# Kernel optimization log

Hardware: AMD Instinct MI355X
Metric: run time of the kernel (lower is better)

The kernel has to match this reference:

```python
import jax, jax.numpy as jnp
import numpy as np

N_USERS = 19968
N_ITEMS = 6144
EMBED = 64
V_DIM = 4096
T_DIM = 384
KNN_K = 10
LAMBDA = 0.9          # lambda_coeff
N_LAYERS = 1          # item-graph propagation layers
N_UI_LAYERS = 2       # len(weight_size)
NNZ = 600000


def build_sim(x):
    # cosine similarity: row-normalize then x @ x.T  -> [N, N]
    xn = x / jnp.linalg.norm(x, axis=-1, keepdims=True)
    return xn @ xn.T


def knn_graph(adj, k):
    # torch.topk + scatter_: keep top-k values per row, zeros elsewhere
    vals, idx = jax.lax.top_k(adj, k)                      # [N, k]
    rows = jnp.arange(adj.shape[0])[:, None]
    return jnp.zeros_like(adj).at[rows, idx].set(vals)


def norm_laplacian(adj):
    # D^{-1/2} A D^{-1/2} with inf -> 0
    d = jnp.sum(adj, axis=-1) ** -0.5
    d = jnp.where(jnp.isinf(d), 0.0, d)
    return adj * d[:, None] * d[None, :]


def setup_inputs() -> dict:
    key = jax.random.key(0)
    ks = jax.random.split(key, 10)
    user_emb = jax.random.normal(ks[0], (N_USERS, EMBED), jnp.float32) * 0.1
    item_emb = jax.random.normal(ks[1], (N_ITEMS, EMBED), jnp.float32) * 0.1
    image_feat = jax.random.normal(ks[2], (N_ITEMS, V_DIM), jnp.float32)
    text_feat = jax.random.normal(ks[3], (N_ITEMS, T_DIM), jnp.float32)
    image_trs_w = jax.random.normal(ks[4], (V_DIM, EMBED), jnp.float32) * 0.02
    image_trs_b = jnp.zeros((EMBED,), jnp.float32)
    text_trs_w = jax.random.normal(ks[5], (T_DIM, EMBED), jnp.float32) * 0.05
    text_trs_b = jnp.zeros((EMBED,), jnp.float32)
    modal_weight = jnp.array([0.5, 0.5], jnp.float32)
    # frozen buffers: knn laplacians built from the raw multimodal features
    image_orig_adj = norm_laplacian(knn_graph(build_sim(image_feat), KNN_K))
    text_orig_adj = norm_laplacian(knn_graph(build_sim(text_feat), KNN_K))
    n_nodes = N_USERS + N_ITEMS
    rows = jax.random.randint(ks[6], (NNZ,), 0, n_nodes, dtype=jnp.int32)
    cols = jax.random.randint(ks[7], (NNZ,), 0, n_nodes, dtype=jnp.int32)
    adj_indices = jnp.stack([rows, cols], axis=0)           # [2, NNZ] COO
    adj_values = jax.random.uniform(ks[8], (NNZ,), jnp.float32) * 0.01
    return {
        "user_emb": user_emb, "item_emb": item_emb,
        "image_feat": image_feat, "text_feat": text_feat,
        "image_trs_w": image_trs_w, "image_trs_b": image_trs_b,
        "text_trs_w": text_trs_w, "text_trs_b": text_trs_b,
        "modal_weight": modal_weight,
        "image_orig_adj": image_orig_adj, "text_orig_adj": text_orig_adj,
        "adj_indices": adj_indices, "adj_values": adj_values,
        "knn_k": KNN_K,
    }


def reference(user_emb, item_emb, image_feat, text_feat,
              image_trs_w, image_trs_b, text_trs_w, text_trs_b,
              modal_weight, image_orig_adj, text_orig_adj,
              adj_indices, adj_values, knn_k):
    # modality projections
    image_feats = image_feat @ image_trs_w + image_trs_b   # [N_items, 64]
    text_feats = text_feat @ text_trs_w + text_trs_b       # [N_items, 64]
    w = jax.nn.softmax(modal_weight)
    # build_item_graph=True branch
    image_adj = knn_graph(build_sim(image_feats), knn_k)
    text_adj = knn_graph(build_sim(text_feats), knn_k)
    learned_adj = norm_laplacian(w[0] * image_adj + w[1] * text_adj)
    original_adj = w[0] * image_orig_adj + w[1] * text_orig_adj
    item_adj = (1.0 - LAMBDA) * learned_adj + LAMBDA * original_adj
    # item-graph propagation
    h = item_emb
    for _ in range(N_LAYERS):
        h = item_adj @ h
    # lightgcn user-item propagation via sparse COO matmul
    ego = jnp.concatenate([user_emb, item_emb], axis=0)    # [n_nodes, 64]
    n_nodes = ego.shape[0]
    src, dst = adj_indices[0], adj_indices[1]
    all_emb = [ego]
    for _ in range(N_UI_LAYERS):
        ego = jax.ops.segment_sum(adj_values[:, None] * ego[dst], src,
                                  num_segments=n_nodes)
        all_emb.append(ego)
    all_emb = jnp.mean(jnp.stack(all_emb, axis=1), axis=1)
    u_g = all_emb[:N_USERS]
    h_norm = h / jnp.maximum(jnp.linalg.norm(h, axis=1, keepdims=True), 1e-12)
    i_g = all_emb[N_USERS:] + h_norm
    return u_g, i_g
```

## Files before the change

### kernel.cpp

```cpp
#include <hip/hip_runtime.h>
#include <hip/hip_bf16.h>

#define NU 19968
#define NI 6144
#define NNODE (NU + NI)
#define EMB 64
#define VD 4096
#define TD 384
#define NNZE 600000
#define LAMB 0.9f
#define NCH 8
#define CPC (NI / NCH)
#define MAXC 16

typedef __attribute__((ext_vector_type(8))) short bf16x8;
typedef __attribute__((ext_vector_type(4))) float f32x4;
#define MFMA16(a, b, c) __builtin_amdgcn_mfma_f32_16x16x32_bf16(a, b, c, 0, 0, 0)


__device__ __forceinline__ void vins(float (&cv)[10], float v) {
#pragma unroll
    for (int s = 0; s < 10; ++s) {
        float mx = fmaxf(cv[s], v);
        v = fminf(cv[s], v);
        cv[s] = mx;
    }
}

__device__ __forceinline__ void topk_ins_tie(float (&cv)[10], int (&ci)[10], float v, int j) {
#pragma unroll
    for (int s = 0; s < 10; ++s) {
        bool take = (v > cv[s]) || (v == cv[s] && j < ci[s]);
        if (take) {
            float tv = cv[s]; cv[s] = v; v = tv;
            int tj = ci[s]; ci[s] = j; j = tj;
        }
    }
}

__device__ __forceinline__ float2 softmax2(const float* mw) {
    float e0 = expf(mw[0]), e1 = expf(mw[1]);
    float inv = 1.0f / (e0 + e1);
    return make_float2(e0 * inv, e1 * inv);
}

__device__ __forceinline__ unsigned short f2bf(float f) {
    unsigned int u = __float_as_uint(f);
    unsigned int r = (u + 0x7FFFu + ((u >> 16) & 1u)) >> 16;
    return (unsigned short)r;
}
__device__ __forceinline__ float bf2f(unsigned short h) { return __uint_as_float(((unsigned int)h) << 16); }

__device__ __forceinline__ f32x4 sim_tile(const unsigned short* __restrict__ xh,
                                          const unsigned short* __restrict__ xl,
                                          bf16x8 ahi0, bf16x8 ahi1, bf16x8 alo0, bf16x8 alo1,
                                          int c, int fq) {
    const size_t bbase = (size_t)c * 64 + fq * 8;
    bf16x8 bhi0 = *(const bf16x8*)(xh + bbase);
    bf16x8 bhi1 = *(const bf16x8*)(xh + bbase + 32);
    bf16x8 blo0 = *(const bf16x8*)(xl + bbase);
    bf16x8 blo1 = *(const bf16x8*)(xl + bbase + 32);
    f32x4 a = {0.f, 0.f, 0.f, 0.f};
    a = MFMA16(ahi0, bhi0, a);
    a = MFMA16(ahi1, bhi1, a);
    a = MFMA16(ahi0, blo0, a);
    a = MFMA16(ahi1, blo1, a);
    a = MFMA16(alo0, bhi0, a);
    a = MFMA16(alo1, bhi1, a);
    return a;
}


__global__ __launch_bounds__(256) void gemm_tr(const float* __restrict__ A, const float* __restrict__ W,
                                               float* __restrict__ C, int M, int K, int kps) {
    __shared__ float At[64][64];
    __shared__ float Wt[64][64];
    const int t = threadIdx.x;
    const int m0 = blockIdx.x * 64;
    const int k0 = blockIdx.y * kps;
    const int tm = t & 15, tn = t >> 4;
    float acc[4][4] = {};
    for (int kt = k0; kt < k0 + kps; kt += 64) {
        __syncthreads();
        for (int i = t; i < 1024; i += 256) {
            int m = i >> 4, k4 = (i & 15) << 2;
            float4 v = *(const float4*)(A + (size_t)(m0 + m) * K + kt + k4);
            At[k4 + 0][m] = v.x; At[k4 + 1][m] = v.y; At[k4 + 2][m] = v.z; At[k4 + 3][m] = v.w;
        }
        for (int i = t; i < 1024; i += 256) {
            int kk = i >> 4, n4 = (i & 15) << 2;
            *(float4*)&Wt[kk][n4] = *(const float4*)(W + (size_t)(kt + kk) * 64 + n4);
        }
        __syncthreads();
#pragma unroll
        for (int kk = 0; kk < 64; ++kk) {
            float a[4], b[4];
            *(float4*)a = *(const float4*)&At[kk][tm << 2];
            *(float4*)b = *(const float4*)&Wt[kk][tn << 2];
#pragma unroll
            for (int i = 0; i < 4; ++i)
#pragma unroll
                for (int j = 0; j < 4; ++j) acc[i][j] += a[i] * b[j];
        }
    }
#pragma unroll
    for (int i = 0; i < 4; ++i)
#pragma unroll
        for (int j = 0; j < 4; ++j)
            unsafeAtomicAdd(&C[(size_t)(m0 + (tm << 2) + i) * 64 + (tn << 2) + j], acc[i][j]);
}


__global__ __launch_bounds__(256) void rownorm(const float* __restrict__ C, const float* __restrict__ bias,
                                               unsigned short* __restrict__ xh, unsigned short* __restrict__ xl) {
    int row = blockIdx.x * 4 + (threadIdx.x >> 6);
    int lane = threadIdx.x & 63;
    float v = C[(size_t)row * 64 + lane] + bias[lane];
    float ss = v * v;
#pragma unroll
    for (int o = 32; o; o >>= 1) ss += __shfl_xor(ss, o, 64);
    float xn = v * (1.0f / sqrtf(ss));
    unsigned short h = f2bf(xn);
    float lo = xn - bf2f(h);
    xh[(size_t)row * 64 + lane] = h;
    xl[(size_t)row * 64 + lane] = f2bf(lo);
}


__global__ __launch_bounds__(256) void sims_tauA(const unsigned short* __restrict__ xh_img,
                                                 const unsigned short* __restrict__ xl_img,
                                                 const unsigned short* __restrict__ xh_txt,
                                                 const unsigned short* __restrict__ xl_txt,
                                                 float* __restrict__ tkv) {
    const unsigned short* xh = blockIdx.z ? xh_txt : xh_img;
    const unsigned short* xl = blockIdx.z ? xl_txt : xl_img;
    const int r0 = blockIdx.x * 64;
    const int c0 = blockIdx.y * CPC;
    const int t = threadIdx.x;
    const int wave = t >> 6, lane = t & 63;
    const int fr = lane & 15, fq = lane >> 4;

    const size_t abase = (size_t)(r0 + wave * 16 + fr) * 64 + fq * 8;
    bf16x8 ahi0 = *(const bf16x8*)(xh + abase);
    bf16x8 ahi1 = *(const bf16x8*)(xh + abase + 32);
    bf16x8 alo0 = *(const bf16x8*)(xl + abase);
    bf16x8 alo1 = *(const bf16x8*)(xl + abase + 32);

    float cv[4][10];
#pragma unroll
    for (int r = 0; r < 4; ++r)
#pragma unroll
        for (int s = 0; s < 10; ++s) cv[r][s] = -INFINITY;

    for (int ct = 0; ct < CPC / 64; ++ct) {
        const int cbase = c0 + ct * 64;
#pragma unroll
        for (int cs = 0; cs < 4; ++cs) {
            f32x4 a = sim_tile(xh, xl, ahi0, ahi1, alo0, alo1, cbase + cs * 16 + fr, fq);
#pragma unroll
            for (int r = 0; r < 4; ++r)
                if (a[r] > cv[r][9]) vins(cv[r], a[r]);
        }
    }

#pragma unroll
    for (int m = 1; m <= 8; m <<= 1) {
#pragma unroll
        for (int r = 0; r < 4; ++r) {
            float ov[10];
#pragma unroll
            for (int s = 0; s < 10; ++s) ov[s] = __shfl_xor(cv[r][s], m);
            bool done = false;
#pragma unroll
            for (int s = 0; s < 10; ++s) {
                if (!done) {
                    if (__all(ov[s] <= cv[r][9])) done = true;
                    else if (ov[s] > cv[r][9]) vins(cv[r], ov[s]);
                }
            }
        }
    }

    if (fr == 0) {
#pragma unroll
        for (int r = 0; r < 4; ++r) {
            int row = r0 + wave * 16 + fq * 4 + r;
            size_t base = ((size_t)(blockIdx.z * NI + row) * NCH + blockIdx.y) * 10;
#pragma unroll
            for (int s = 0; s < 10; ++s) tkv[base + s] = cv[r][s];
        }
    }
}


__global__ void tau_merge(const float* __restrict__ tkv, float* __restrict__ tau) {
    int g = blockIdx.x * blockDim.x + threadIdx.x;
    if (g >= 2 * NI) return;
    float cv[10];
#pragma unroll
    for (int s = 0; s < 10; ++s) cv[s] = -INFINITY;
    for (int u = 0; u < NCH * 10; ++u) {
        float v = tkv[(size_t)g * NCH * 10 + u];
        if (v > cv[9]) vins(cv, v);
    }
    tau[g] = cv[9];
}


__global__ __launch_bounds__(256) void sims_collect(const unsigned short* __restrict__ xh_img,
                                                    const unsigned short* __restrict__ xl_img,
                                                    const unsigned short* __restrict__ xh_txt,
                                                    const unsigned short* __restrict__ xl_txt,
                                                    const float* __restrict__ tau,
                                                    int* __restrict__ ccnt,
                                                    float* __restrict__ cval, int* __restrict__ ccol) {
    const unsigned short* xh = blockIdx.z ? xh_txt : xh_img;
    const unsigned short* xl = blockIdx.z ? xl_txt : xl_img;
    const int r0 = blockIdx.x * 64;
    const int c0 = blockIdx.y * CPC;
    const int t = threadIdx.x;
    const int wave = t >> 6, lane = t & 63;
    const int fr = lane & 15, fq = lane >> 4;

    const size_t abase = (size_t)(r0 + wave * 16 + fr) * 64 + fq * 8;
    bf16x8 ahi0 = *(const bf16x8*)(xh + abase);
    bf16x8 ahi1 = *(const bf16x8*)(xh + abase + 32);
    bf16x8 alo0 = *(const bf16x8*)(xl + abase);
    bf16x8 alo1 = *(const bf16x8*)(xl + abase + 32);

    float tv[4];
    int grow[4];
#pragma unroll
    for (int r = 0; r < 4; ++r) {
        grow[r] = blockIdx.z * NI + r0 + wave * 16 + fq * 4 + r;
        tv[r] = tau[grow[r]];
    }

    for (int ct = 0; ct < CPC / 64; ++ct) {
        const int cbase = c0 + ct * 64;
#pragma unroll
        for (int cs = 0; cs < 4; ++cs) {
            const int c = cbase + cs * 16 + fr;
            f32x4 a = sim_tile(xh, xl, ahi0, ahi1, alo0, alo1, c, fq);
#pragma unroll
            for (int r = 0; r < 4; ++r) {
                if (a[r] >= tv[r]) {
                    int p = atomicAdd(&ccnt[grow[r]], 1);
                    if (p < MAXC) {
                        cval[(size_t)grow[r] * MAXC + p] = a[r];
                        ccol[(size_t)grow[r] * MAXC + p] = c;
                    }
                }
            }
        }
    }
}


__global__ void topk_cand(const int* __restrict__ ccnt, const float* __restrict__ cval,
                          const int* __restrict__ ccol,
                          float* __restrict__ fvv, int* __restrict__ fii) {
    int g = blockIdx.x * blockDim.x + threadIdx.x;
    if (g >= 2 * NI) return;
    float cv[10]; int ci[10];
#pragma unroll
    for (int s = 0; s < 10; ++s) { cv[s] = -INFINITY; ci[s] = 0x7fffffff; }
    int n = ccnt[g]; if (n > MAXC) n = MAXC;
    for (int u = 0; u < n; ++u)
        topk_ins_tie(cv, ci, cval[(size_t)g * MAXC + u], ccol[(size_t)g * MAXC + u]);
#pragma unroll
    for (int s = 0; s < 10; ++s) { fvv[(size_t)g * 10 + s] = cv[s]; fii[(size_t)g * 10 + s] = ci[s]; }
}


__global__ void calc_dinv(const float* __restrict__ fvv, const float* __restrict__ mw, float* __restrict__ dinv) {
    int i = blockIdx.x * blockDim.x + threadIdx.x;
    if (i >= NI) return;
    float2 w = softmax2(mw);
    float s = 0.f;
    for (int u = 0; u < 10; ++u) s += w.x * fvv[(size_t)i * 10 + u];
    for (int u = 0; u < 10; ++u) s += w.y * fvv[(size_t)(NI + i) * 10 + u];
    dinv[i] = (s > 0.f) ? (1.0f / sqrtf(s)) : 0.f;
}


__global__ __launch_bounds__(256) void compute_h(const float* __restrict__ img_o, const float* __restrict__ txt_o,
                                                 const float* __restrict__ item_emb,
                                                 const float* __restrict__ fvv, const int* __restrict__ fii,
                                                 const float* __restrict__ dinv, const float* __restrict__ mw,
                                                 float* __restrict__ hnorm) {
    const int i = blockIdx.x;
    const int t = threadIdx.x;
    __shared__ int   sj[64];
    __shared__ float sc[64];
    __shared__ int   scnt;
    __shared__ float part[4][64];
    if (t == 0) scnt = 0;
    __syncthreads();
    float2 w = softmax2(mw);
    const float4* ro = (const float4*)(img_o + (size_t)i * NI);
    const float4* to = (const float4*)(txt_o + (size_t)i * NI);
    for (int u = t; u < NI / 4; u += 256) {
        float4 a = ro[u], b = to[u];
        float c[4] = { w.x * a.x + w.y * b.x, w.x * a.y + w.y * b.y,
                       w.x * a.z + w.y * b.z, w.x * a.w + w.y * b.w };
#pragma unroll
        for (int q = 0; q < 4; ++q)
            if (c[q] != 0.f) { int p = atomicAdd(&scnt, 1); sj[p] = u * 4 + q; sc[p] = LAMB * c[q]; }
    }
    if (t < 20) {
        int m = t / 10, s = t % 10;
        float v = fvv[((size_t)m * NI + i) * 10 + s];
        int   j = fii[((size_t)m * NI + i) * 10 + s];
        float wm = m ? w.y : w.x;
        float c = (1.0f - LAMB) * wm * v * dinv[i] * dinv[j];
        int p = atomicAdd(&scnt, 1); sj[p] = j; sc[p] = c;
    }
    __syncthreads();
    const int cnt = scnt;
    const int dim = t & 63, q = t >> 6;
    float acc = 0.f;
    for (int e = q; e < cnt; e += 4) acc += sc[e] * item_emb[(size_t)sj[e] * 64 + dim];
    part[q][dim] = acc;
    __syncthreads();
    if (t < 64) {
        float h = part[0][t] + part[1][t] + part[2][t] + part[3][t];
        float ss = h * h;
#pragma unroll
        for (int o = 32; o; o >>= 1) ss += __shfl_xor(ss, o, 64);
        float scale = 1.0f / fmaxf(sqrtf(ss), 1e-12f);
        hnorm[(size_t)i * 64 + t] = h * scale;
    }
}


__global__ void hist_k(const int* __restrict__ aidx, int* __restrict__ cnt) {
    int e = blockIdx.x * 256 + threadIdx.x;
    if (e < NNZE) atomicAdd(&cnt[aidx[e]], 1);
}

__global__ void scan_partial(const int* __restrict__ cnt, int* __restrict__ rp, int* __restrict__ partials) {
    __shared__ int sm[256];
    int t = threadIdx.x;
    int i = blockIdx.x * 256 + t;
    int v = cnt[i];
    sm[t] = v;
    __syncthreads();
    for (int o = 1; o < 256; o <<= 1) {
        int x = (t >= o) ? sm[t - o] : 0;
        __syncthreads();
        sm[t] += x;
        __syncthreads();
    }
    rp[i] = sm[t] - v;
    if (t == 255) partials[blockIdx.x] = sm[255];
}

__global__ void scan_totals(int* __restrict__ partials, int* __restrict__ rp) {
    if (threadIdx.x == 0) {
        int s = 0;
        for (int b = 0; b < NNODE / 256; ++b) { int v = partials[b]; partials[b] = s; s += v; }
        rp[NNODE] = s;
    }
}

__global__ void add_off(int* __restrict__ rp, const int* __restrict__ partials, int* __restrict__ fill) {
    int i = blockIdx.x * 256 + threadIdx.x;
    int v = rp[i] + partials[blockIdx.x];
    rp[i] = v;
    fill[i] = v;
}

__global__ void scatter_k(const int* __restrict__ aidx, const float* __restrict__ avals,
                          int* __restrict__ fill, int* __restrict__ cdst, float* __restrict__ cval) {
    int e = blockIdx.x * 256 + threadIdx.x;
    if (e >= NNZE) return;
    int src = aidx[e];
    int p = atomicAdd(&fill[src], 1);
    cdst[p] = aidx[NNZE + e];
    cval[p] = avals[e];
}


__global__ __launch_bounds__(256) void ui_gather(const float* __restrict__ uin, const float* __restrict__ iin,
                                                 const float* __restrict__ full_in,
                                                 const int* __restrict__ rp, const int* __restrict__ cdst,
                                                 const float* __restrict__ cval, float* __restrict__ out) {
    int row = blockIdx.x * 4 + (threadIdx.x >> 6);
    int lane = threadIdx.x & 63;
    int s = rp[row], e = rp[row + 1];
    float acc = 0.f;
    int p = s;
    for (; p + 2 <= e; p += 2) {
        int d0 = cdst[p], d1 = cdst[p + 1];
        float v0 = cval[p], v1 = cval[p + 1];
        const float* r0 = full_in ? full_in + (size_t)d0 * 64
                                  : (d0 < NU ? uin + (size_t)d0 * 64 : iin + (size_t)(d0 - NU) * 64);
        const float* r1 = full_in ? full_in + (size_t)d1 * 64
                                  : (d1 < NU ? uin + (size_t)d1 * 64 : iin + (size_t)(d1 - NU) * 64);
        acc += v0 * r0[lane];
        acc += v1 * r1[lane];
    }
    if (p < e) {
        int d0 = cdst[p]; float v0 = cval[p];
        const float* r0 = full_in ? full_in + (size_t)d0 * 64
                                  : (d0 < NU ? uin + (size_t)d0 * 64 : iin + (size_t)(d0 - NU) * 64);
        acc += v0 * r0[lane];
    }
    out[(size_t)row * 64 + lane] = acc;
}


__global__ __launch_bounds__(256) void final_out(const float* __restrict__ ue, const float* __restrict__ ie,
                                                 const float* __restrict__ e1, const float* __restrict__ e2,
                                                 const float* __restrict__ hnorm, float* __restrict__ out) {
    int g = blockIdx.x * 256 + threadIdx.x;
    if (g >= NNODE * 16) return;
    int n = g >> 4;
    float4 a = (n < NU) ? ((const float4*)ue)[g] : ((const float4*)ie)[g - NU * 16];
    float4 b = ((const float4*)e1)[g];
    float4 c = ((const float4*)e2)[g];
    const float third = 1.0f / 3.0f;
    float4 r;
    r.x = (a.x + b.x + c.x) * third;
    r.y = (a.y + b.y + c.y) * third;
    r.z = (a.z + b.z + c.z) * third;
    r.w = (a.w + b.w + c.w) * third;
    if (n >= NU) {
        float4 h = ((const float4*)hnorm)[g - NU * 16];
        r.x += h.x; r.y += h.y; r.z += h.z; r.w += h.w;
    }
    ((float4*)out)[g] = r;
}


extern "C" void kernel_launch(void* const* d_in, const int* in_sizes, int n_in,
                              void* d_out, int out_size, void* d_ws, size_t ws_size,
                              hipStream_t stream) {
    const float* user_emb   = (const float*)d_in[0];
    const float* item_emb   = (const float*)d_in[1];
    const float* image_feat = (const float*)d_in[2];
    const float* text_feat  = (const float*)d_in[3];
    const float* img_w      = (const float*)d_in[4];
    const float* img_b      = (const float*)d_in[5];
    const float* txt_w      = (const float*)d_in[6];
    const float* txt_b      = (const float*)d_in[7];
    const float* mw         = (const float*)d_in[8];
    const float* img_orig   = (const float*)d_in[9];
    const float* txt_orig   = (const float*)d_in[10];
    const int*   aidx       = (const int*)d_in[11];
    const float* avals      = (const float*)d_in[12];

    float* C_img = (float*)d_ws;
    float* C_txt = C_img + (size_t)NI * EMB;
    unsigned short* xh_img = (unsigned short*)(C_txt + (size_t)NI * EMB);
    unsigned short* xl_img = xh_img + (size_t)NI * EMB;
    unsigned short* xh_txt = xl_img + (size_t)NI * EMB;
    unsigned short* xl_txt = xh_txt + (size_t)NI * EMB;
    float* tkvA    = (float*)(xl_txt + (size_t)NI * EMB);
    float* tau     = tkvA + (size_t)2 * NI * NCH * 10;
    int*   ccnt    = (int*)(tau + 2 * NI);
    float* candv   = (float*)(ccnt + 2 * NI);
    int*   candc   = (int*)(candv + (size_t)2 * NI * MAXC);
    float* fin_val = (float*)(candc + (size_t)2 * NI * MAXC);
    int*   fin_idx = (int*)(fin_val + 2 * NI * 10);
    float* dinv    = (float*)(fin_idx + 2 * NI * 10);
    float* hnorm   = dinv + NI;
    float* ego1    = hnorm + (size_t)NI * EMB;
    float* ego2    = ego1 + (size_t)NNODE * EMB;
    int* cnt      = (int*)(ego2 + (size_t)NNODE * EMB);
    int* row_ptr  = cnt + NNODE;
    int* fill     = row_ptr + NNODE + 1;
    int* partials = fill + NNODE;
    int* csr_dst  = partials + 128;
    float* csr_val = (float*)(csr_dst + NNZE);

    hipMemsetAsync(C_img, 0, (size_t)NI * EMB * 4, stream);
    hipMemsetAsync(C_txt, 0, (size_t)NI * EMB * 4, stream);
    hipMemsetAsync(cnt, 0, (size_t)NNODE * 4, stream);
    hipMemsetAsync(ccnt, 0, (size_t)2 * NI * 4, stream);

    hist_k<<<(NNZE + 255) / 256, 256, 0, stream>>>(aidx, cnt);
    scan_partial<<<NNODE / 256, 256, 0, stream>>>(cnt, row_ptr, partials);
    scan_totals<<<1, 64, 0, stream>>>(partials, row_ptr);
    add_off<<<NNODE / 256, 256, 0, stream>>>(row_ptr, partials, fill);
    scatter_k<<<(NNZE + 255) / 256, 256, 0, stream>>>(aidx, avals, fill, csr_dst, csr_val);

    gemm_tr<<<dim3(NI / 64, 8), 256, 0, stream>>>(image_feat, img_w, C_img, NI, VD, VD / 8);
    gemm_tr<<<dim3(NI / 64, 6), 256, 0, stream>>>(text_feat,  txt_w, C_txt, NI, TD, TD / 6);

    rownorm<<<NI / 4, 256, 0, stream>>>(C_img, img_b, xh_img, xl_img);
    rownorm<<<NI / 4, 256, 0, stream>>>(C_txt, txt_b, xh_txt, xl_txt);

    sims_tauA<<<dim3(NI / 64, NCH, 2), 256, 0, stream>>>(xh_img, xl_img, xh_txt, xl_txt, tkvA);
    tau_merge<<<(2 * NI + 255) / 256, 256, 0, stream>>>(tkvA, tau);
    sims_collect<<<dim3(NI / 64, NCH, 2), 256, 0, stream>>>(xh_img, xl_img, xh_txt, xl_txt,
                                                            tau, ccnt, candv, candc);
    topk_cand<<<(2 * NI + 255) / 256, 256, 0, stream>>>(ccnt, candv, candc, fin_val, fin_idx);

    calc_dinv<<<(NI + 255) / 256, 256, 0, stream>>>(fin_val, mw, dinv);

    compute_h<<<NI, 256, 0, stream>>>(img_orig, txt_orig, item_emb, fin_val, fin_idx, dinv, mw, hnorm);

    ui_gather<<<NNODE / 4, 256, 0, stream>>>(user_emb, item_emb, nullptr, row_ptr, csr_dst, csr_val, ego1);
    ui_gather<<<NNODE / 4, 256, 0, stream>>>(user_emb, item_emb, ego1,    row_ptr, csr_dst, csr_val, ego2);

    final_out<<<(NNODE * 16 + 255) / 256, 256, 0, stream>>>(user_emb, item_emb, ego1, ego2, hnorm, (float*)d_out);
}
```

Measured before the change: 1.034 ms.

## Use split-bf16 MFMA projection GEMM, vectorize sparse gather, parallelize scan

Replaces the fp32 FMA projection GEMM with an MFMA kernel that splits inputs into bf16 hi/lo parts and computes three products. Each K-split now writes its own partial buffer that rownorm sums, which removes the atomics and memsets. The sparse user-item gather uses float4 loads across four edge groups with a shuffle reduction, and the serial scan_totals becomes a shared-memory parallel scan. It also doubles the similarity column chunks (NCH) and aliases workspace buffers, at the cost of slightly lower GEMM precision and more tau-merge work.

```diff
diff --git a/kernel.cpp b/kernel.cpp
--- a/kernel.cpp
+++ b/kernel.cpp
@@ -9,7 +9,7 @@
 #define TD 384
 #define NNZE 600000
 #define LAMB 0.9f
-#define NCH 8
+#define NCH 16
 #define CPC (NI / NCH)
 #define MAXC 16
 
@@ -71,51 +71,75 @@
 }
 
 
-__global__ __launch_bounds__(256) void gemm_tr(const float* __restrict__ A, const float* __restrict__ W,
-                                               float* __restrict__ C, int M, int K, int kps) {
-    __shared__ float At[64][64];
-    __shared__ float Wt[64][64];
+__global__ __launch_bounds__(256) void gemm_mfma(const float* __restrict__ A, const float* __restrict__ W,
+                                                 float* __restrict__ Cp, int K, int kps) {
+    __shared__ unsigned short Ah[64][72], Al[64][72], Wh[64][72], Wl[64][72];
     const int t = threadIdx.x;
     const int m0 = blockIdx.x * 64;
     const int k0 = blockIdx.y * kps;
-    const int tm = t & 15, tn = t >> 4;
-    float acc[4][4] = {};
+    const int wv = t >> 6, lane = t & 63;
+    const int fr = lane & 15, fq = lane >> 4;
+    f32x4 acc[4] = {{0,0,0,0},{0,0,0,0},{0,0,0,0},{0,0,0,0}};
     for (int kt = k0; kt < k0 + kps; kt += 64) {
         __syncthreads();
-        for (int i = t; i < 1024; i += 256) {
+#pragma unroll
+        for (int q = 0; q < 4; ++q) {
+            int i = t + 256 * q;
             int m = i >> 4, k4 = (i & 15) << 2;
             float4 v = *(const float4*)(A + (size_t)(m0 + m) * K + kt + k4);
-            At[k4 + 0][m] = v.x; At[k4 + 1][m] = v.y; At[k4 + 2][m] = v.z; At[k4 + 3][m] = v.w;
-        }
-        for (int i = t; i < 1024; i += 256) {
+            float f[4] = {v.x, v.y, v.z, v.w};
+#pragma unroll
+            for (int j = 0; j < 4; ++j) {
+                unsigned short h = f2bf(f[j]);
+                Ah[m][k4 + j] = h;
+                Al[m][k4 + j] = f2bf(f[j] - bf2f(h));
+            }
+        }
+#pragma unroll
+        for (int q = 0; q < 4; ++q) {
+            int i = t + 256 * q;
             int kk = i >> 4, n4 = (i & 15) << 2;
-            *(float4*)&Wt[kk][n4] = *(const float4*)(W + (size_t)(kt + kk) * 64 + n4);
+            float4 v = *(const float4*)(W + (size_t)(kt + kk) * 64 + n4);
+            float f[4] = {v.x, v.y, v.z, v.w};
+#pragma unroll
+            for (int j = 0; j < 4; ++j) {
+                unsigned short h = f2bf(f[j]);
+                Wh[n4 + j][kk] = h;
+                Wl[n4 + j][kk] = f2bf(f[j] - bf2f(h));
+            }
         }
         __syncthreads();
 #pragma unroll
-        for (int kk = 0; kk < 64; ++kk) {
-            float a[4], b[4];
-            *(float4*)a = *(const float4*)&At[kk][tm << 2];
-            *(float4*)b = *(const float4*)&Wt[kk][tn << 2];
-#pragma unroll
-            for (int i = 0; i < 4; ++i)
-#pragma unroll
-                for (int j = 0; j < 4; ++j) acc[i][j] += a[i] * b[j];
-        }
-    }
-#pragma unroll
-    for (int i = 0; i < 4; ++i)
-#pragma unroll
-        for (int j = 0; j < 4; ++j)
-            unsafeAtomicAdd(&C[(size_t)(m0 + (tm << 2) + i) * 64 + (tn << 2) + j], acc[i][j]);
-}
-
-
-__global__ __launch_bounds__(256) void rownorm(const float* __restrict__ C, const float* __restrict__ bias,
-                                               unsigned short* __restrict__ xh, unsigned short* __restrict__ xl) {
+        for (int k2 = 0; k2 < 2; ++k2) {
+            bf16x8 ah = *(const bf16x8*)&Ah[wv * 16 + fr][k2 * 32 + fq * 8];
+            bf16x8 al = *(const bf16x8*)&Al[wv * 16 + fr][k2 * 32 + fq * 8];
+#pragma unroll
+            for (int cs = 0; cs < 4; ++cs) {
+                bf16x8 wh = *(const bf16x8*)&Wh[cs * 16 + fr][k2 * 32 + fq * 8];
+                bf16x8 wl = *(const bf16x8*)&Wl[cs * 16 + fr][k2 * 32 + fq * 8];
+                acc[cs] = MFMA16(ah, wh, acc[cs]);
+                acc[cs] = MFMA16(ah, wl, acc[cs]);
+                acc[cs] = MFMA16(al, wh, acc[cs]);
+            }
+        }
+    }
+    const size_t base = (size_t)blockIdx.y * NI * 64;
+#pragma unroll
+    for (int cs = 0; cs < 4; ++cs)
+#pragma unroll
+        for (int r = 0; r < 4; ++r)
+            Cp[base + (size_t)(m0 + wv * 16 + fq * 4 + r) * 64 + cs * 16 + fr] = acc[cs][r];
+}
+
+
+__global__ __launch_bounds__(256) void rownorm(const float* __restrict__ Cp, const float* __restrict__ bias,
+                                               unsigned short* __restrict__ xh, unsigned short* __restrict__ xl,
+                                               int ns) {
     int row = blockIdx.x * 4 + (threadIdx.x >> 6);
     int lane = threadIdx.x & 63;
-    float v = C[(size_t)row * 64 + lane] + bias[lane];
+    float v = 0.f;
+    for (int s = 0; s < ns; ++s) v += Cp[((size_t)s * NI + row) * 64 + lane];
+    v += bias[lane];
     float ss = v * v;
 #pragma unroll
     for (int o = 32; o; o >>= 1) ss += __shfl_xor(ss, o, 64);
@@ -357,11 +381,20 @@
 }
 
 __global__ void scan_totals(int* __restrict__ partials, int* __restrict__ rp) {
-    if (threadIdx.x == 0) {
-        int s = 0;
-        for (int b = 0; b < NNODE / 256; ++b) { int v = partials[b]; partials[b] = s; s += v; }
-        rp[NNODE] = s;
-    }
+    __shared__ int sm[128];
+    int t = threadIdx.x;
+    const int NB = NNODE / 256;
+    int v = (t < NB) ? partials[t] : 0;
+    sm[t] = v;
+    __syncthreads();
+    for (int o = 1; o < 128; o <<= 1) {
+        int x = (t >= o) ? sm[t - o] : 0;
+        __syncthreads();
+        sm[t] += x;
+        __syncthreads();
+    }
+    if (t < NB) partials[t] = sm[t] - v;
+    if (t == 127) rp[NNODE] = sm[127];
 }
 
 __global__ void add_off(int* __restrict__ rp, const int* __restrict__ partials, int* __restrict__ fill) {
@@ -388,26 +421,25 @@
                                                  const float* __restrict__ cval, float* __restrict__ out) {
     int row = blockIdx.x * 4 + (threadIdx.x >> 6);
     int lane = threadIdx.x & 63;
+    int g16 = lane & 15, egrp = lane >> 4;
     int s = rp[row], e = rp[row + 1];
-    float acc = 0.f;
-    int p = s;
-    for (; p + 2 <= e; p += 2) {
-        int d0 = cdst[p], d1 = cdst[p + 1];
-        float v0 = cval[p], v1 = cval[p + 1];
-        const float* r0 = full_in ? full_in + (size_t)d0 * 64
-                                  : (d0 < NU ? uin + (size_t)d0 * 64 : iin + (size_t)(d0 - NU) * 64);
-        const float* r1 = full_in ? full_in + (size_t)d1 * 64
-                                  : (d1 < NU ? uin + (size_t)d1 * 64 : iin + (size_t)(d1 - NU) * 64);
-        acc += v0 * r0[lane];
-        acc += v1 * r1[lane];
-    }
-    if (p < e) {
-        int d0 = cdst[p]; float v0 = cval[p];
-        const float* r0 = full_in ? full_in + (size_t)d0 * 64
-                                  : (d0 < NU ? uin + (size_t)d0 * 64 : iin + (size_t)(d0 - NU) * 64);
-        acc += v0 * r0[lane];
-    }
-    out[(size_t)row * 64 + lane] = acc;
+    float4 acc = {0.f, 0.f, 0.f, 0.f};
+    for (int p = s + egrp; p < e; p += 4) {
+        int d = cdst[p];
+        float v = cval[p];
+        const float* r0 = full_in ? full_in + (size_t)d * 64
+                                  : (d < NU ? uin + (size_t)d * 64 : iin + (size_t)(d - NU) * 64);
+        float4 x = *(const float4*)(r0 + g16 * 4);
+        acc.x += v * x.x; acc.y += v * x.y; acc.z += v * x.z; acc.w += v * x.w;
+    }
+#pragma unroll
+    for (int m = 16; m <= 32; m <<= 1) {
+        acc.x += __shfl_xor(acc.x, m, 64);
+        acc.y += __shfl_xor(acc.y, m, 64);
+        acc.z += __shfl_xor(acc.z, m, 64);
+        acc.w += __shfl_xor(acc.w, m, 64);
+    }
+    if (egrp == 0) *(float4*)(out + (size_t)row * 64 + g16 * 4) = acc;
 }
 
 
@@ -451,14 +483,19 @@
     const int*   aidx       = (const int*)d_in[11];
     const float* avals      = (const float*)d_in[12];
 
-    float* C_img = (float*)d_ws;
-    float* C_txt = C_img + (size_t)NI * EMB;
-    unsigned short* xh_img = (unsigned short*)(C_txt + (size_t)NI * EMB);
+    float* R = (float*)d_ws;
+    float* Cp_img = R;
+    float* Cp_txt = R + 3145728;
+    float* tkvA   = R + 3145728 + 2359296;
+    float* ego1   = R;
+    float* ego2   = R + 1671168;
+
+    float* after = R + 7471104;
+    unsigned short* xh_img = (unsigned short*)after;
     unsigned short* xl_img = xh_img + (size_t)NI * EMB;
     unsigned short* xh_txt = xl_img + (size_t)NI * EMB;
     unsigned short* xl_txt = xh_txt + (size_t)NI * EMB;
-    float* tkvA    = (float*)(xl_txt + (size_t)NI * EMB);
-    float* tau     = tkvA + (size_t)2 * NI * NCH * 10;
+    float* tau     = (float*)(xl_txt + (size_t)NI * EMB);
     int*   ccnt    = (int*)(tau + 2 * NI);
     float* candv   = (float*)(ccnt + 2 * NI);
     int*   candc   = (int*)(candv + (size_t)2 * NI * MAXC);
@@ -466,31 +503,27 @@
     int*   fin_idx = (int*)(fin_val + 2 * NI * 10);
     float* dinv    = (float*)(fin_idx + 2 * NI * 10);
     float* hnorm   = dinv + NI;
-    float* ego1    = hnorm + (size_t)NI * EMB;
-    float* ego2    = ego1 + (size_t)NNODE * EMB;
-    int* cnt      = (int*)(ego2 + (size_t)NNODE * EMB);
+    int* cnt      = (int*)(hnorm + (size_t)NI * EMB);
     int* row_ptr  = cnt + NNODE;
     int* fill     = row_ptr + NNODE + 1;
     int* partials = fill + NNODE;
     int* csr_dst  = partials + 128;
     float* csr_val = (float*)(csr_dst + NNZE);
 
-    hipMemsetAsync(C_img, 0, (size_t)NI * EMB * 4, stream);
-    hipMemsetAsync(C_txt, 0, (size_t)NI * EMB * 4, stream);
     hipMemsetAsync(cnt, 0, (size_t)NNODE * 4, stream);
     hipMemsetAsync(ccnt, 0, (size_t)2 * NI * 4, stream);
 
     hist_k<<<(NNZE + 255) / 256, 256, 0, stream>>>(aidx, cnt);
     scan_partial<<<NNODE / 256, 256, 0, stream>>>(cnt, row_ptr, partials);
-    scan_totals<<<1, 64, 0, stream>>>(partials, row_ptr);
+    scan_totals<<<1, 128, 0, stream>>>(partials, row_ptr);
     add_off<<<NNODE / 256, 256, 0, stream>>>(row_ptr, partials, fill);
     scatter_k<<<(NNZE + 255) / 256, 256, 0, stream>>>(aidx, avals, fill, csr_dst, csr_val);
 
-    gemm_tr<<<dim3(NI / 64, 8), 256, 0, stream>>>(image_feat, img_w, C_img, NI, VD, VD / 8);
-    gemm_tr<<<dim3(NI / 64, 6), 256, 0, stream>>>(text_feat,  txt_w, C_txt, NI, TD, TD / 6);
-
-    rownorm<<<NI / 4, 256, 0, stream>>>(C_img, img_b, xh_img, xl_img);
-    rownorm<<<NI / 4, 256, 0, stream>>>(C_txt, txt_b, xh_txt, xl_txt);
+    gemm_mfma<<<dim3(NI / 64, 8), 256, 0, stream>>>(image_feat, img_w, Cp_img, VD, VD / 8);
+    gemm_mfma<<<dim3(NI / 64, 6), 256, 0, stream>>>(text_feat,  txt_w, Cp_txt, TD, TD / 6);
+
+    rownorm<<<NI / 4, 256, 0, stream>>>(Cp_img, img_b, xh_img, xl_img, 8);
+    rownorm<<<NI / 4, 256, 0, stream>>>(Cp_txt, txt_b, xh_txt, xl_txt, 6);
 
     sims_tauA<<<dim3(NI / 64, NCH, 2), 256, 0, stream>>>(xh_img, xl_img, xh_txt, xl_txt, tkvA);
     tau_merge<<<(2 * NI + 255) / 256, 256, 0, stream>>>(tkvA, tau);
```

Result: faster. 984.5 us (-4.8%).
